# Kernel optimization log

Hardware: AMD Instinct MI355X
Metric: run time of the kernel (lower is better)

## Reference

```python
import jax, jax.numpy as jnp
import numpy as np

N, S_CT, D = 64, 128, 1024
WIN = 5
EPS = 1e-8
STOP = 0.1
MAX_DEPTH = 25


def layer_norm(x, g, b, eps=1e-5):
    mu = jnp.mean(x, axis=-1, keepdims=True)
    var = jnp.var(x, axis=-1, keepdims=True)
    return (x - mu) / jnp.sqrt(var + eps) * g + b


def _augment(sequence, input_mask, START, END):
    n, s, d = sequence.shape
    seq = jnp.concatenate([jnp.broadcast_to(START, (n, 1, d)), sequence], axis=1)
    m = jnp.concatenate([jnp.ones((n, 1, 1), seq.dtype), input_mask], axis=1)
    m_no_end = jnp.concatenate([m, jnp.zeros((n, 1, 1), seq.dtype)], axis=1)
    m_yes_end = jnp.concatenate([jnp.ones((n, 1, 1), seq.dtype), m], axis=1)
    end_mask = m_yes_end - m_no_end  # one-hot at END slot
    seq = jnp.concatenate([seq, jnp.zeros((n, 1, d), seq.dtype)], axis=1)
    seq = end_mask * END + (1.0 - end_mask) * seq
    m_no_start = jnp.concatenate([jnp.zeros((n, 1, 1), seq.dtype), m_yes_end[:, 1:]], axis=1)
    return seq, m_yes_end, end_mask, m_no_start, m_no_end


def _neighbor_probs(exist_probs, mask):
    # exist_probs, mask: (n,s,1). Returns left/right soft-neighbor matrices (n,s,s).
    n, s, _ = mask.shape
    m = jnp.stack([mask[:, ::-1, 0], mask[:, :, 0]], axis=1)            # (n,2,s)
    p = jnp.stack([exist_probs[:, ::-1, 0], exist_probs[:, :, 0]], axis=1)
    tri = jnp.triu(jnp.ones((s, s), mask.dtype), k=1)
    mat = (p * m)[:, :, None, :] * tri                                   # (n,2,s,s)
    cs = jnp.cumsum(mat, axis=-1)
    rem_left = jnp.concatenate([jnp.ones((n, 2, s, 1), mask.dtype), 1.0 - cs[..., :-1]], axis=-1)
    rem_left = jnp.maximum(rem_left, 0.0)
    right = jnp.where(cs > 1.0, rem_left, mat) * m[:, :, None, :]
    left = jnp.flip(right[:, 0], axis=(1, 2))
    return left, right[:, 1]


def crvnn_forward(sequence, input_mask, START, END, W_conv, b_conv, W_scorer, b_scorer,
                  W_init, b_init, W_cell1, b_cell1, W_cell2, b_cell2,
                  ln1_g, ln1_b, ln2_g, ln2_b):
    seq, mask, end_mask, m_no_start, m_no_end = _augment(sequence, input_mask, START, END)
    n, s, d = seq.shape
    last_mask = jnp.concatenate([end_mask[:, 1:], jnp.zeros((n, 1, 1), seq.dtype)], axis=1)
    sel_mask = m_no_start * m_no_end * (1.0 - last_mask)  # start_end_last_mask
    seq = layer_norm((seq * mask) @ W_init + b_init, ln1_g, ln1_b) * mask
    exist = jnp.ones((n, s, 1), seq.dtype) * mask

    def step(carry, _):
        sq, ep, um = carry
        L, R = _neighbor_probs(ep, mask)
        l1 = L @ sq; l2 = L @ l1
        r1 = R @ sq; r2 = R @ r1
        win = jnp.concatenate([l2, l1, sq, r1, r2], axis=-1)  # (n,s,5d) == stacked window flattened
        h = jax.nn.gelu(win @ W_conv + b_conv, approximate=False)
        sc = h @ W_scorer + b_scorer                           # (n,s,1) transition score
        scores = jnp.concatenate([sc, jnp.zeros_like(sc)], axis=-1)
        exp_scores = jnp.exp(scores - jnp.max(scores))
        exp_t = exp_scores[..., 0:1] * sel_mask
        exp_n = exp_scores[..., 1:2]
        # sum_normalize over {transition, no_op}; gate halted samples via um (tp=0 => no-op)
        tp = exp_t / (exp_t + exp_n + 2.0 * EPS) * um[:, None, None]
        # compose(left_child, self)
        cat = jnp.concatenate([l1, sq], axis=-1)
        hid = jax.nn.gelu(cat @ W_cell1 + b_cell1, approximate=False)
        contents = (hid @ W_cell2 + b_cell2).reshape(n, s, 4, d)
        gates = jax.nn.sigmoid(contents[:, :, 0:3, :])
        comp = layer_norm(gates[:, :, 0] * l1 + gates[:, :, 1] * sq + gates[:, :, 2] * contents[:, :, 3, :], ln2_g, ln2_b)
        new_sq = tp * comp + (1.0 - tp) * sq
        new_ep = ep * (1.0 - (R @ tp))  # left neighbor consumed with prob of right neighbor transition
        active = jnp.sum(new_ep * sel_mask, axis=(1, 2))
        new_um = um * (active >= STOP).astype(sq.dtype)
        return (new_sq, new_ep, new_um), None

    steps = min(s - 2, MAX_DEPTH)
    (seq, exist, _), _ = jax.lax.scan(step, (seq, exist, jnp.ones((n,), seq.dtype)), None, length=steps)
    seq = seq * mask
    global_state = jnp.sum(last_mask * seq, axis=1)  # root lands at last content slot
    return seq[:, 1:-1, :], global_state


def setup_inputs():
    key = jax.random.key(0)
    ks = jax.random.split(key, 8)
    sc = 0.02
    f32 = jnp.float32
    return {
        "sequence": jax.random.normal(ks[0], (N, S_CT, D), f32),
        "input_mask": jnp.ones((N, S_CT, 1), f32),
        "START": jax.random.normal(ks[1], (D,), f32),
        "END": jax.random.normal(ks[2], (D,), f32),
        "W_conv": jax.random.normal(ks[3], (WIN * D, D), f32) * sc,
        "b_conv": jnp.zeros((D,), f32),
        "W_scorer": jax.random.normal(ks[4], (D, 1), f32) * sc,
        "b_scorer": jnp.zeros((1,), f32),
        "W_init": jax.random.normal(ks[5], (D, D), f32) * sc,
        "b_init": jnp.zeros((D,), f32),
        "W_cell1": jax.random.normal(ks[6], (2 * D, 4 * D), f32) * sc,
        "b_cell1": jnp.zeros((4 * D,), f32),
        "W_cell2": jax.random.normal(ks[7], (4 * D, 4 * D), f32) * sc,
        "b_cell2": jnp.zeros((4 * D,), f32),
        "ln1_g": jnp.ones((D,), f32), "ln1_b": jnp.zeros((D,), f32),
        "ln2_g": jnp.ones((D,), f32), "ln2_b": jnp.zeros((D,), f32),
    }


def reference(sequence, input_mask, START, END, W_conv, b_conv, W_scorer, b_scorer,
              W_init, b_init, W_cell1, b_cell1, W_cell2, b_cell2,
              ln1_g, ln1_b, ln2_g, ln2_b):
    return crvnn_forward(sequence, input_mask, START, END, W_conv, b_conv, W_scorer, b_scorer,
                         W_init, b_init, W_cell1, b_cell1, W_cell2, b_cell2,
                         ln1_g, ln1_b, ln2_g, ln2_b)
```

## Files before the change

kernel.cpp:

```cpp
#include <hip/hip_runtime.h>
#include <math.h>


#define NB 64
#define SS 130
#define DD 1024
#define MM (NB*SS)
#define LSTR 132
#define CROWS 1664

typedef _Float16 f16x8 __attribute__((ext_vector_type(8)));
typedef _Float16 f16x4 __attribute__((ext_vector_type(4)));
typedef _Float16 f16x2 __attribute__((ext_vector_type(2)));
typedef float f32x4 __attribute__((ext_vector_type(4)));

struct GemmSrc { const float* a[5]; };

__device__ __forceinline__ float bsum(float v){
  __shared__ float sh[4];
  __syncthreads();
  #pragma unroll
  for (int o=32;o;o>>=1) v += __shfl_down(v,o);
  if ((threadIdx.x & 63)==0) sh[threadIdx.x>>6] = v;
  __syncthreads();
  return sh[0]+sh[1]+sh[2]+sh[3];
}
__device__ __forceinline__ float bmaxr(float v){
  __shared__ float sh[4];
  __syncthreads();
  #pragma unroll
  for (int o=32;o;o>>=1) v = fmaxf(v,__shfl_down(v,o));
  if ((threadIdx.x & 63)==0) sh[threadIdx.x>>6] = v;
  __syncthreads();
  return fmaxf(fmaxf(sh[0],sh[1]),fmaxf(sh[2],sh[3]));
}
__device__ __forceinline__ float gelu_(float x){
  return 0.5f*x*(1.f+erff(x*0.70710678118654752f));
}

__global__ __launch_bounds__(256) void build_masks(
    const float* __restrict__ im, float* __restrict__ mk, float* __restrict__ sel,
    float* __restrict__ lastm, float* __restrict__ endm, float* __restrict__ ep,
    float* __restrict__ um, int* __restrict__ flag){
  int b = blockIdx.x, i = threadIdx.x;
  if (i < SS){
    float mye = (i<=1) ? 1.f : im[b*128 + (i-2)];
    float mne = (i==SS-1) ? 0.f : ((i==0) ? 1.f : im[b*128 + (i-1)]);
    float em  = mye - mne;
    float mns = (i==0) ? 0.f : mye;
    float lm;
    if (i < SS-1){
      int i1 = i+1;
      float mye1 = (i1<=1) ? 1.f : im[b*128 + (i1-2)];
      float mne1 = (i1==SS-1) ? 0.f : im[b*128 + (i1-1)];
      lm = mye1 - mne1;
    } else lm = 0.f;
    float sl = mns * mne * (1.f - lm);
    int idx = b*SS + i;
    mk[idx]=mye; sel[idx]=sl; lastm[idx]=lm; endm[idx]=em; ep[idx]=mye;
  } else if (i == SS) { um[b] = 1.f; }
  else if (i == SS+1 && b==0) { flag[0] = 0; }
}

__global__ __launch_bounds__(256) void build_seq(
    const float* __restrict__ seqin, const float* __restrict__ START,
    const float* __restrict__ END, const float* __restrict__ mk,
    const float* __restrict__ endm, float* __restrict__ out){
  int r = blockIdx.x; int b = r/SS, i = r%SS; int t = threadIdx.x;
  float em = endm[r], m = mk[r];
  #pragma unroll
  for (int q=0;q<4;q++){
    int j = t + q*256;
    float v;
    if (i==0) v = START[j];
    else if (i<=128) v = seqin[((size_t)b*128 + (i-1))*DD + j];
    else v = 0.f;
    v = em*END[j] + (1.f-em)*v;
    out[(size_t)r*DD + j] = v*m;
  }
}

__global__ __launch_bounds__(256) void wtranspose(
    const float* __restrict__ W, _Float16* __restrict__ WTh, _Float16* __restrict__ WTl,
    int K, int N){
  __shared__ float Ts[32][33];
  int k0 = blockIdx.x*32, n0 = blockIdx.y*32;
  int t = threadIdx.x;
  int r = t>>3, c4 = (t&7)*4;
  float4 v = *(const float4*)(W + (size_t)(k0+r)*N + n0 + c4);
  Ts[r][c4]=v.x; Ts[r][c4+1]=v.y; Ts[r][c4+2]=v.z; Ts[r][c4+3]=v.w;
  __syncthreads();
  int n = t>>3, k4 = (t&7)*4;
  f16x4 h, lo;
  #pragma unroll
  for (int i=0;i<4;i++){
    float xs = Ts[k4+i][n] * 64.f;
    _Float16 hh = (_Float16)xs;
    h[i] = hh; lo[i] = (_Float16)((xs - (float)hh) * 2048.f);
  }
  *(f16x4*)(WTh + (size_t)(n0+n)*K + k0+k4) = h;
  *(f16x4*)(WTl + (size_t)(n0+n)*K + k0+k4) = lo;
}

template<bool PRE>
__global__ __launch_bounds__(256,2) void gemm_mfma(
    GemmSrc S, long lda,
    const _Float16* __restrict__ WTh, const _Float16* __restrict__ WTl,
    const float* __restrict__ Wf, int Nw,
    const float* __restrict__ bias,
    float* __restrict__ C, long ldc, int K, int act,
    const int* __restrict__ flag, float* __restrict__ spart, const float* __restrict__ Ws){
  if (flag[0]) return;
  __shared__ _Float16 Ah[128][40], Al[128][40];
  __shared__ _Float16 Wh[128][40], Wl[128][40];
  const int t = threadIdx.x;
  const int wave = t >> 6, lane = t & 63;
  const int wm = wave >> 1, wn = wave & 1;
  const int l15 = lane & 15, l4 = lane >> 4;
  int lin = blockIdx.y * gridDim.x + blockIdx.x;
  int nwg = gridDim.x * gridDim.y;
  int q = nwg >> 3, r = nwg & 7;
  int xcd = lin & 7, pos = lin >> 3;
  int wg = (xcd < r) ? (xcd*(q+1) + pos) : (r*(q+1) + (xcd - r)*q + pos);
  int MT = gridDim.y;
  int mt = wg % MT, nt = wg / MT;
  const long mb = (long)mt * 128;
  const int  nb = nt * 128;
  f32x4 accH[4][4], accX[4][4];
  #pragma unroll
  for (int i=0;i<4;i++)
    #pragma unroll
    for (int j=0;j<4;j++){ accH[i][j] = (f32x4){0.f,0.f,0.f,0.f}; accX[i][j] = (f32x4){0.f,0.f,0.f,0.f}; }

  for (int kt=0; kt<K; kt+=32){
    #pragma unroll
    for (int p=0;p<4;p++){
      int f = t + 256*p;
      int m = f >> 3;
      int k4 = (f & 7) * 4;
      int kg = kt + k4;
      const float* src = S.a[kg >> 10];
      float4 v = *(const float4*)(src + (mb + m)*lda + (kg & 1023));
      f16x4 h, lo;
      _Float16 hh;
      hh=(_Float16)v.x; h[0]=hh; lo[0]=(_Float16)((v.x-(float)hh)*2048.f);
      hh=(_Float16)v.y; h[1]=hh; lo[1]=(_Float16)((v.y-(float)hh)*2048.f);
      hh=(_Float16)v.z; h[2]=hh; lo[2]=(_Float16)((v.z-(float)hh)*2048.f);
      hh=(_Float16)v.w; h[3]=hh; lo[3]=(_Float16)((v.w-(float)hh)*2048.f);
      *(f16x4*)&Ah[m][k4] = h;
      *(f16x4*)&Al[m][k4] = lo;
    }
    if constexpr (PRE){
      #pragma unroll
      for (int p=0;p<2;p++){
        int f = t + 256*p;
        int n = f >> 2;
        int ko = (f & 3) * 8;
        *(f16x8*)&Wh[n][ko] = *(const f16x8*)(WTh + (size_t)(nb + n)*K + kt + ko);
        *(f16x8*)&Wl[n][ko] = *(const f16x8*)(WTl + (size_t)(nb + n)*K + kt + ko);
      }
    } else {
      #pragma unroll
      for (int p=0;p<2;p++){
        int u = t + 256*p;
        int kp = u >> 5;
        int c  = u & 31;
        const float* wsrc = Wf + (size_t)(kt + 2*kp)*Nw + nb + c;
        #pragma unroll
        for (int i=0;i<4;i++){
          float x0 = wsrc[32*i] * 64.f;
          float x1 = wsrc[(size_t)Nw + 32*i] * 64.f;
          _Float16 h0 = (_Float16)x0, h1 = (_Float16)x1;
          _Float16 g0 = (_Float16)((x0 - (float)h0)*2048.f);
          _Float16 g1 = (_Float16)((x1 - (float)h1)*2048.f);
          f16x2 hp; hp[0]=h0; hp[1]=h1;
          f16x2 lp; lp[0]=g0; lp[1]=g1;
          int n = c + 32*i;
          *(f16x2*)&Wh[n][2*kp] = hp;
          *(f16x2*)&Wl[n][2*kp] = lp;
        }
      }
    }
    __syncthreads();
    f16x8 wh[4], wl[4];
    #pragma unroll
    for (int i=0;i<4;i++){
      wh[i] = *(const f16x8*)&Wh[wn*64 + i*16 + l15][8*l4];
      wl[i] = *(const f16x8*)&Wl[wn*64 + i*16 + l15][8*l4];
    }
    #pragma unroll
    for (int mi=0;mi<4;mi++){
      f16x8 ahv = *(const f16x8*)&Ah[wm*64 + mi*16 + l15][8*l4];
      f16x8 alv = *(const f16x8*)&Al[wm*64 + mi*16 + l15][8*l4];
      #pragma unroll
      for (int ni=0;ni<4;ni++){
        accH[mi][ni] = __builtin_amdgcn_mfma_f32_16x16x32_f16(wh[ni], ahv, accH[mi][ni], 0,0,0);
        accX[mi][ni] = __builtin_amdgcn_mfma_f32_16x16x32_f16(wh[ni], alv, accX[mi][ni], 0,0,0);
        accX[mi][ni] = __builtin_amdgcn_mfma_f32_16x16x32_f16(wl[ni], ahv, accX[mi][ni], 0,0,0);
      }
    }
    __syncthreads();
  }

  const float IH = 1.f/64.f, IX = 1.f/131072.f;
  if (act==2){
    #pragma unroll
    for (int mi=0;mi<4;mi++){
      float s = 0.f;
      #pragma unroll
      for (int ni=0;ni<4;ni++){
        int nbase = nb + wn*64 + ni*16 + 4*l4;
        #pragma unroll
        for (int rr=0;rr<4;rr++){
          float v = gelu_(accH[mi][ni][rr]*IH + accX[mi][ni][rr]*IX + bias[nbase+rr]);
          s = fmaf(v, Ws[nbase+rr], s);
        }
      }
      s += __shfl_xor(s, 16);
      s += __shfl_xor(s, 32);
      if (l4==0){
        long m = mb + wm*64 + mi*16 + l15;
        spart[m*16 + nt*2 + wn] = s;
      }
    }
    return;
  }
  #pragma unroll
  for (int mi=0;mi<4;mi++){
    long m = mb + wm*64 + mi*16 + l15;
    #pragma unroll
    for (int ni=0;ni<4;ni++){
      int nbase = nb + wn*64 + ni*16 + 4*l4;
      float4 v;
      v.x = accH[mi][ni][0]*IH + accX[mi][ni][0]*IX + bias[nbase+0];
      v.y = accH[mi][ni][1]*IH + accX[mi][ni][1]*IX + bias[nbase+1];
      v.z = accH[mi][ni][2]*IH + accX[mi][ni][2]*IX + bias[nbase+2];
      v.w = accH[mi][ni][3]*IH + accX[mi][ni][3]*IX + bias[nbase+3];
      if (act==1){ v.x=gelu_(v.x); v.y=gelu_(v.y); v.z=gelu_(v.z); v.w=gelu_(v.w); }
      *(float4*)(C + m*ldc + nbase) = v;
    }
  }
}

__global__ __launch_bounds__(256,2) void gemm_f32(
    GemmSrc S, long lda, const float* __restrict__ B, const float* __restrict__ bias,
    float* __restrict__ C, long ldc, int N, int K, int act,
    const int* __restrict__ flag){
  if (flag[0]) return;
  __shared__ float Asm[16][132];
  __shared__ float Bsm[16][132];
  float acc[8][8];
  #pragma unroll
  for (int i=0;i<8;i++)
    #pragma unroll
    for (int j=0;j<8;j++) acc[i][j]=0.f;
  const int t = threadIdx.x;
  const int tx = t & 15, ty = t >> 4;
  const long mb = (long)blockIdx.y * 128;
  const int  nb = blockIdx.x * 128;
  for (int kt=0; kt<K; kt+=16){
    #pragma unroll
    for (int ii=0; ii<2; ii++){
      int f  = t + 256*ii;
      int m  = f >> 2;
      int k4 = (f & 3) * 4;
      int kg = kt + k4;
      const float* src = S.a[kg >> 10];
      float4 v = *(const float4*)(src + (mb + m)*lda + (kg & 1023));
      Asm[k4+0][m]=v.x; Asm[k4+1][m]=v.y; Asm[k4+2][m]=v.z; Asm[k4+3][m]=v.w;
    }
    #pragma unroll
    for (int ii=0; ii<2; ii++){
      int f  = t + 256*ii;
      int kk = f >> 5;
      int c4 = (f & 31)*4;
      *(float4*)&Bsm[kk][c4] = *(const float4*)(B + (long)(kt+kk)*N + nb + c4);
    }
    __syncthreads();
    #pragma unroll
    for (int kk=0;kk<16;kk++){
      float av[8], bv[8];
      *(float4*)&av[0] = *(const float4*)&Asm[kk][ty*4];
      *(float4*)&av[4] = *(const float4*)&Asm[kk][64+ty*4];
      *(float4*)&bv[0] = *(const float4*)&Bsm[kk][tx*4];
      *(float4*)&bv[4] = *(const float4*)&Bsm[kk][64+tx*4];
      #pragma unroll
      for (int r=0;r<8;r++)
        #pragma unroll
        for (int c=0;c<8;c++) acc[r][c] = fmaf(av[r],bv[c],acc[r][c]);
    }
    __syncthreads();
  }
  #pragma unroll
  for (int rh=0;rh<2;rh++)
  #pragma unroll
  for (int rr=0;rr<4;rr++){
    long row = mb + rh*64 + ty*4 + rr;
    #pragma unroll
    for (int ch=0;ch<2;ch++){
      int col = nb + ch*64 + tx*4;
      float t0 = acc[rh*4+rr][ch*4+0] + bias[col+0];
      float t1 = acc[rh*4+rr][ch*4+1] + bias[col+1];
      float t2 = acc[rh*4+rr][ch*4+2] + bias[col+2];
      float t3 = acc[rh*4+rr][ch*4+3] + bias[col+3];
      if (act==1){ t0=gelu_(t0); t1=gelu_(t1); t2=gelu_(t2); t3=gelu_(t3); }
      float4 v; v.x=t0; v.y=t1; v.z=t2; v.w=t3;
      *(float4*)(C + row*ldc + col) = v;
    }
  }
}

__global__ __launch_bounds__(256,2) void bgemm(
    const float* __restrict__ P, const float* __restrict__ X, float* __restrict__ Y,
    const int* __restrict__ flag){
  if (flag[0]) return;
  __shared__ float Ps[64][17];
  __shared__ float Xs[16][132];
  const int t = threadIdx.x;
  const int nt = blockIdx.x, mt = blockIdx.y, b = blockIdx.z;
  const int i0 = mt*64;
  const float* Pb = P + (size_t)b*SS*LSTR;
  const float* Xb = X + (size_t)b*SS*DD + nt*128;
  float* Yb = Y + (size_t)b*SS*DD + nt*128;
  const int tx = t & 7, ty = t >> 3;
  float acc[2][16];
  #pragma unroll
  for (int r=0;r<2;r++)
    #pragma unroll
    for (int c=0;c<16;c++) acc[r][c]=0.f;
  for (int j0=0;j0<SS;j0+=16){
    { int r = t>>2, c0 = (t&3)*4;
      float4 v = make_float4(0.f,0.f,0.f,0.f);
      if (i0 + r < SS && j0 + c0 < LSTR) v = *(const float4*)(Pb + (size_t)(i0+r)*LSTR + j0 + c0);
      Ps[r][c0]=v.x; Ps[r][c0+1]=v.y; Ps[r][c0+2]=v.z; Ps[r][c0+3]=v.w;
    }
    #pragma unroll
    for (int ii=0;ii<2;ii++){
      int f = t + 256*ii;
      int jj = f>>5, c4 = (f&31)*4;
      float4 v = make_float4(0.f,0.f,0.f,0.f);
      if (j0 + jj < SS) v = *(const float4*)(Xb + (size_t)(j0+jj)*DD + c4);
      *(float4*)&Xs[jj][c4] = v;
    }
    __syncthreads();
    #pragma unroll
    for (int jj=0;jj<16;jj++){
      float p0 = Ps[2*ty][jj], p1 = Ps[2*ty+1][jj];
      #pragma unroll
      for (int q=0;q<4;q++){
        float4 xv = *(const float4*)&Xs[jj][tx*4 + 32*q];
        acc[0][q*4+0] = fmaf(p0,xv.x,acc[0][q*4+0]);
        acc[0][q*4+1] = fmaf(p0,xv.y,acc[0][q*4+1]);
        acc[0][q*4+2] = fmaf(p0,xv.z,acc[0][q*4+2]);
        acc[0][q*4+3] = fmaf(p0,xv.w,acc[0][q*4+3]);
        acc[1][q*4+0] = fmaf(p1,xv.x,acc[1][q*4+0]);
        acc[1][q*4+1] = fmaf(p1,xv.y,acc[1][q*4+1]);
        acc[1][q*4+2] = fmaf(p1,xv.z,acc[1][q*4+2]);
        acc[1][q*4+3] = fmaf(p1,xv.w,acc[1][q*4+3]);
      }
    }
    __syncthreads();
  }
  #pragma unroll
  for (int rr=0;rr<2;rr++){
    int row = i0 + 2*ty + rr;
    if (row < SS){
      #pragma unroll
      for (int q=0;q<4;q++){
        float4 v = make_float4(acc[rr][q*4],acc[rr][q*4+1],acc[rr][q*4+2],acc[rr][q*4+3]);
        *(float4*)(Yb + (size_t)row*DD + tx*4 + 32*q) = v;
      }
    }
  }
}

__global__ void neighbor_kernel(const float* __restrict__ ep, const float* __restrict__ mk,
                                float* __restrict__ L, float* __restrict__ R,
                                const int* __restrict__ flag){
  if (flag[0]) return;
  int idx = blockIdx.x*blockDim.x + threadIdx.x;
  if (idx >= MM) return;
  int b = idx / SS, i = idx % SS;
  const float* p = ep + b*SS;
  const float* m = mk + b*SS;
  float* Lr = L + (size_t)idx*LSTR;
  float* Rr = R + (size_t)idx*LSTR;
  for (int j=0;j<LSTR;j++){ Lr[j]=0.f; Rr[j]=0.f; }
  float cs=0.f;
  for (int j=i+1;j<SS;j++){
    float mat = p[j]*m[j];
    cs += mat;
    float v = (cs>1.f) ? fmaxf(1.f-(cs-mat),0.f) : mat;
    Rr[j] = v*m[j];
  }
  cs=0.f;
  for (int j=i-1;j>=0;j--){
    float mat = p[j]*m[j];
    cs += mat;
    float v = (cs>1.f) ? fmaxf(1.f-(cs-mat),0.f) : mat;
    Lr[j] = v*m[j];
  }
}

__global__ __launch_bounds__(256) void ln1_kernel(
    const float* __restrict__ xin, const float* __restrict__ g, const float* __restrict__ bb,
    const float* __restrict__ mk, float* __restrict__ out){
  int r = blockIdx.x, t = threadIdx.x;
  const float* xr = xin + (size_t)r*DD;
  float x[4]; float s=0.f;
  #pragma unroll
  for (int q=0;q<4;q++){ x[q]=xr[t+256*q]; s+=x[q]; }
  float mean = bsum(s)*(1.f/DD);
  float vs=0.f;
  #pragma unroll
  for (int q=0;q<4;q++){ float d=x[q]-mean; vs+=d*d; }
  float var = bsum(vs)*(1.f/DD);
  float inv = 1.f/sqrtf(var+1e-5f);
  float m = mk[r];
  #pragma unroll
  for (int q=0;q<4;q++){ int j=t+256*q; out[(size_t)r*DD+j] = ((x[q]-mean)*inv*g[j]+bb[j])*m; }
}

__global__ void scorer_final(const float* __restrict__ spart, const float* __restrict__ bs,
                             float* __restrict__ sc, const int* __restrict__ flag){
  if (flag[0]) return;
  int r = blockIdx.x*blockDim.x + threadIdx.x;
  if (r >= MM) return;
  float s = bs[0];
  #pragma unroll
  for (int k=0;k<16;k++) s += spart[(size_t)r*16+k];
  sc[r] = s;
}
__global__ __launch_bounds__(256) void max1(const float* __restrict__ sc, float* __restrict__ part,
                                            const int* __restrict__ flag){
  if (flag[0]) return;
  int idx = blockIdx.x*256 + threadIdx.x;
  float v = -1e30f;
  for (int i = idx; i < MM; i += 64*256) v = fmaxf(v, sc[i]);
  v = bmaxr(v);
  if (threadIdx.x==0) part[blockIdx.x] = v;
}
__global__ __launch_bounds__(64) void max2(const float* __restrict__ part, float* __restrict__ gm,
                                           const int* __restrict__ flag){
  if (flag[0]) return;
  float v = part[threadIdx.x];
  #pragma unroll
  for (int o=32;o;o>>=1) v = fmaxf(v, __shfl_down(v,o));
  if (threadIdx.x==0) gm[0] = fmaxf(v, 0.f);
}
__global__ void tp_kernel(const float* __restrict__ sc, const float* __restrict__ sel,
                          const float* __restrict__ um, const float* __restrict__ gm,
                          float* __restrict__ tp, const int* __restrict__ flag){
  if (flag[0]) return;
  int idx = blockIdx.x*blockDim.x + threadIdx.x;
  if (idx>=MM) return;
  int b = idx / SS;
  float g = gm[0];
  float et = expf(sc[idx]-g)*sel[idx];
  float en = expf(-g);
  tp[idx] = et/(et+en+2e-8f)*um[b];
}

__global__ __launch_bounds__(256) void update_kernel(
    const float* __restrict__ cont, const float* __restrict__ l1, float* __restrict__ sq,
    const float* __restrict__ tp, const float* __restrict__ g, const float* __restrict__ bb,
    const int* __restrict__ flag, long row0){
  if (flag[0]) return;
  long r = row0 + blockIdx.x; int t = threadIdx.x;
  const float* cr = cont + (size_t)blockIdx.x*4096;
  const float* lr = l1 + (size_t)r*DD;
  float* sr = sq + (size_t)r*DD;
  float x[4], sv[4];
  float s=0.f;
  #pragma unroll
  for (int q=0;q<4;q++){
    int j = t+q*256;
    float c0=cr[j], c1=cr[DD+j], c2=cr[2*DD+j], c3=cr[3*DD+j];
    float g0=1.f/(1.f+expf(-c0));
    float g1=1.f/(1.f+expf(-c1));
    float g2=1.f/(1.f+expf(-c2));
    float lv=lr[j]; float sqv=sr[j]; sv[q]=sqv;
    x[q] = g0*lv + g1*sqv + g2*c3;
    s += x[q];
  }
  float mean = bsum(s)*(1.f/DD);
  float vs=0.f;
  #pragma unroll
  for (int q=0;q<4;q++){ float d=x[q]-mean; vs+=d*d; }
  float var = bsum(vs)*(1.f/DD);
  float inv = 1.f/sqrtf(var+1e-5f);
  float tpv = tp[r];
  #pragma unroll
  for (int q=0;q<4;q++){
    int j=t+q*256;
    float comp = (x[q]-mean)*inv*g[j]+bb[j];
    sr[j] = tpv*comp + (1.f-tpv)*sv[q];
  }
}

__global__ void ep_update(float* __restrict__ ep, const float* __restrict__ R,
                          const float* __restrict__ tp, const int* __restrict__ flag){
  if (flag[0]) return;
  int idx = blockIdx.x*blockDim.x + threadIdx.x;
  if (idx>=MM) return;
  int b = idx / SS;
  const float* Rr = R + (size_t)idx*LSTR;
  const float* tb = tp + b*SS;
  float d=0.f;
  for (int j=0;j<SS;j++) d = fmaf(Rr[j],tb[j],d);
  ep[idx] *= (1.f - d);
}
__global__ __launch_bounds__(256) void active_um(const float* __restrict__ ep,
                                                 const float* __restrict__ sel,
                                                 float* __restrict__ um,
                                                 const int* __restrict__ flag){
  if (flag[0]) return;
  int b = blockIdx.x, t = threadIdx.x;
  float s = (t<SS) ? ep[b*SS+t]*sel[b*SS+t] : 0.f;
  s = bsum(s);
  if (t==0) um[b] *= (s >= 0.1f) ? 1.f : 0.f;
}
__global__ __launch_bounds__(64) void done_kernel(const float* __restrict__ um, int* __restrict__ flag){
  float v = um[threadIdx.x];
  unsigned long long b = __ballot(v > 0.f);
  if (threadIdx.x==0) flag[0] = (b==0ULL) ? 1 : 0;
}

__global__ __launch_bounds__(256) void output_kernel(const float* __restrict__ sq,
                                                     const float* __restrict__ mk,
                                                     float* __restrict__ out){
  int r = blockIdx.x; int b = r/SS, i = r%SS;
  if (i<1 || i>128) return;
  float m = mk[r]; int t=threadIdx.x;
  #pragma unroll
  for (int q=0;q<4;q++){
    int j = t+q*256;
    out[((size_t)b*128 + (i-1))*DD + j] = sq[(size_t)r*DD + j]*m;
  }
}
__global__ __launch_bounds__(256) void gstate_kernel(const float* __restrict__ sq,
                                                     const float* __restrict__ mk,
                                                     const float* __restrict__ lastm,
                                                     float* __restrict__ outg){
  int b = blockIdx.x; int t=threadIdx.x;
  #pragma unroll
  for (int q=0;q<4;q++){
    int j = t+q*256;
    float acc=0.f;
    for (int i=0;i<SS;i++){
      float w = lastm[b*SS+i]*mk[b*SS+i];
      acc = fmaf(w, sq[((size_t)(b*SS+i))*DD + j], acc);
    }
    outg[(size_t)b*DD + j] = acc;
  }
}

extern "C" void kernel_launch(void* const* d_in, const int* in_sizes, int n_in,
                              void* d_out, int out_size, void* d_ws, size_t ws_size,
                              hipStream_t stream) {
  const float* sequence   = (const float*)d_in[0];
  const float* input_mask = (const float*)d_in[1];
  const float* START      = (const float*)d_in[2];
  const float* END        = (const float*)d_in[3];
  const float* W_conv     = (const float*)d_in[4];
  const float* b_conv     = (const float*)d_in[5];
  const float* W_scorer   = (const float*)d_in[6];
  const float* b_scorer   = (const float*)d_in[7];
  const float* W_init     = (const float*)d_in[8];
  const float* b_init     = (const float*)d_in[9];
  const float* W_cell1    = (const float*)d_in[10];
  const float* b_cell1    = (const float*)d_in[11];
  const float* W_cell2    = (const float*)d_in[12];
  const float* b_cell2    = (const float*)d_in[13];
  const float* ln1g       = (const float*)d_in[14];
  const float* ln1b       = (const float*)d_in[15];
  const float* ln2g       = (const float*)d_in[16];
  const float* ln2b       = (const float*)d_in[17];

  float* ws = (float*)d_ws;
  const size_t U = (size_t)MM*DD;
  float* sq   = ws;
  float* l1   = ws + U;
  float* r1   = ws + 2*U;
  float* l2   = ws + 3*U;
  float* r2   = ws + 4*U;
  float* Lm   = ws + 5*U;
  float* Rm   = Lm + (size_t)NB*SS*LSTR;
  float* maskv= Rm + (size_t)NB*SS*LSTR;
  float* sel  = maskv + MM;
  float* lastm= sel + MM;
  float* endm = lastm + MM;
  float* ep   = endm + MM;
  float* scb  = ep + MM;
  float* tpb  = scb + MM;
  float* spart= tpb + MM;
  float* umb  = spart + (size_t)MM*16;
  float* part = umb + NB;
  float* gmx  = part + 64;
  int*   flag = (int*)(gmx + 4);
  size_t used_floats = (size_t)((float*)(flag+4) - ws);
  used_floats = (used_floats + 7) & ~(size_t)7;
  const size_t SC = (size_t)1024*5120, S1 = (size_t)4096*2048, S2 = (size_t)4096*4096;
  _Float16* WT2_h = (_Float16*)(ws + used_floats);
  _Float16* WT2_l = WT2_h + S2;
  _Float16* WT1_h = WT2_l + S2;
  _Float16* WT1_l = WT1_h + S1;
  _Float16* WTc_h = WT1_l + S1;
  _Float16* WTc_l = WTc_h + SC;
  const bool pre2 = ws_size >= (size_t)((char*)(WT2_l + S2) - (char*)d_ws);
  const bool pre1 = ws_size >= (size_t)((char*)(WT1_l + S1) - (char*)d_ws);
  const bool prec = ws_size >= (size_t)((char*)(WTc_l + SC) - (char*)d_ws);

  build_masks<<<NB,256,0,stream>>>(input_mask, maskv, sel, lastm, endm, ep, umb, flag);
  build_seq<<<MM,256,0,stream>>>(sequence, START, END, maskv, endm, r1);
  GemmSrc si; si.a[0]=r1; si.a[1]=r1; si.a[2]=r1; si.a[3]=r1; si.a[4]=r1;
  gemm_f32<<<dim3(8,65),256,0,stream>>>(si, DD, W_init, b_init, l2, DD, DD, DD, 0, flag);
  ln1_kernel<<<MM,256,0,stream>>>(l2, ln1g, ln1b, maskv, sq);

  if (pre2) wtranspose<<<dim3(128,128),256,0,stream>>>(W_cell2, WT2_h, WT2_l, 4096, 4096);
  if (pre1) wtranspose<<<dim3(64,128),256,0,stream>>>(W_cell1, WT1_h, WT1_l, 2048, 4096);
  if (prec) wtranspose<<<dim3(160,32),256,0,stream>>>(W_conv,  WTc_h, WTc_l, 5120, 1024);

  for (int it=0; it<25; ++it){
    neighbor_kernel<<<(MM+255)/256,256,0,stream>>>(ep, maskv, Lm, Rm, flag);
    bgemm<<<dim3(8,3,NB),256,0,stream>>>(Lm, sq, l1, flag);
    bgemm<<<dim3(8,3,NB),256,0,stream>>>(Rm, sq, r1, flag);
    bgemm<<<dim3(8,3,NB),256,0,stream>>>(Lm, l1, l2, flag);
    bgemm<<<dim3(8,3,NB),256,0,stream>>>(Rm, r1, r2, flag);
    GemmSrc s5; s5.a[0]=l2; s5.a[1]=l1; s5.a[2]=sq; s5.a[3]=r1; s5.a[4]=r2;
    if (prec)
      gemm_mfma<true ><<<dim3(8,65),256,0,stream>>>(s5, DD, WTc_h, WTc_l, nullptr, 0, b_conv, nullptr, 0, 5120, 2, flag, spart, W_scorer);
    else
      gemm_mfma<false><<<dim3(8,65),256,0,stream>>>(s5, DD, nullptr, nullptr, W_conv, 1024, b_conv, nullptr, 0, 5120, 2, flag, spart, W_scorer);
    scorer_final<<<(MM+255)/256,256,0,stream>>>(spart, b_scorer, scb, flag);
    max1<<<64,256,0,stream>>>(scb, part, flag);
    max2<<<1,64,0,stream>>>(part, gmx, flag);
    tp_kernel<<<(MM+255)/256,256,0,stream>>>(scb, sel, umb, gmx, tpb, flag);
    for (int c=0;c<5;c++){
      long row0 = (long)c*CROWS;
      GemmSrc s2; s2.a[0]=l1+row0*DD; s2.a[1]=sq+row0*DD; s2.a[2]=s2.a[1]; s2.a[3]=s2.a[1]; s2.a[4]=s2.a[1];
      GemmSrc s3; s3.a[0]=l2; s3.a[1]=l2+DD; s3.a[2]=l2+2*DD; s3.a[3]=l2+3*DD; s3.a[4]=l2;
      if (pre1)
        gemm_mfma<true ><<<dim3(32,13),256,0,stream>>>(s2, DD,   WT1_h, WT1_l, nullptr, 0, b_cell1, l2, 4096, 2048, 1, flag, nullptr, nullptr);
      else
        gemm_mfma<false><<<dim3(32,13),256,0,stream>>>(s2, DD,   nullptr, nullptr, W_cell1, 4096, b_cell1, l2, 4096, 2048, 1, flag, nullptr, nullptr);
      if (pre2)
        gemm_mfma<true ><<<dim3(32,13),256,0,stream>>>(s3, 4096, WT2_h, WT2_l, nullptr, 0, b_cell2, r2, 4096, 4096, 0, flag, nullptr, nullptr);
      else
        gemm_mfma<false><<<dim3(32,13),256,0,stream>>>(s3, 4096, nullptr, nullptr, W_cell2, 4096, b_cell2, r2, 4096, 4096, 0, flag, nullptr, nullptr);
      update_kernel<<<CROWS,256,0,stream>>>(r2, l1, sq, tpb, ln2g, ln2b, flag, row0);
    }
    ep_update<<<(MM+255)/256,256,0,stream>>>(ep, Rm, tpb, flag);
    active_um<<<NB,256,0,stream>>>(ep, sel, umb, flag);
    done_kernel<<<1,64,0,stream>>>(umb, flag);
  }

  float* out = (float*)d_out;
  output_kernel<<<MM,256,0,stream>>>(sq, maskv, out);
  gstate_kernel<<<NB,256,0,stream>>>(sq, maskv, lastm, out + (size_t)NB*128*DD);
}
```

Measured before the change: 67.42 ms.

## Store activations as pre-split fp16 hi/lo pairs and parallelize neighbor/ep kernels

Intermediate activations (sq, l1, r1, l2, r2) are now kept as split fp16 high/low pairs, so the MFMA GEMMs load them straight into shared memory instead of converting fp32 to hi/lo on every K tile. Producers (ln1, bgemm, cell1 GEMM epilogue, update) encode on write, and consumers decode where fp32 is still needed. Separately, neighbor_kernel and ep_update now use one wave per row with shuffle prefix sums and reductions, replacing the serial per-thread loops. The split encoding should keep accuracy close to fp32, but it adds encode/decode work in the bgemm, update and output kernels.

```diff
diff --git a/kernel.cpp b/kernel.cpp
--- a/kernel.cpp
+++ b/kernel.cpp
@@ -8,13 +8,17 @@
 #define MM (NB*SS)
 #define LSTR 132
 #define CROWS 1664
+#define RSC 2048.0f
+#define IRS (1.0f/2048.0f)
 
 typedef _Float16 f16x8 __attribute__((ext_vector_type(8)));
 typedef _Float16 f16x4 __attribute__((ext_vector_type(4)));
 typedef _Float16 f16x2 __attribute__((ext_vector_type(2)));
 typedef float f32x4 __attribute__((ext_vector_type(4)));
 
-struct GemmSrc { const float* a[5]; };
+struct GemmSrcF { const float* a[5]; };
+struct GemmSrcP { const _Float16* h[5]; const _Float16* l[5]; };
+struct hl2 { _Float16 h, l; };
 
 __device__ __forceinline__ float bsum(float v){
   __shared__ float sh[4];
@@ -36,6 +40,12 @@
 }
 __device__ __forceinline__ float gelu_(float x){
   return 0.5f*x*(1.f+erff(x*0.70710678118654752f));
+}
+__device__ __forceinline__ hl2 enc(float x){
+  hl2 r;
+  r.h = (_Float16)x;
+  r.l = (_Float16)((x - (float)r.h)*RSC);
+  return r;
 }
 
 __global__ __launch_bounds__(256) void build_masks(
@@ -94,21 +104,21 @@
   f16x4 h, lo;
   #pragma unroll
   for (int i=0;i<4;i++){
-    float xs = Ts[k4+i][n] * 64.f;
-    _Float16 hh = (_Float16)xs;
-    h[i] = hh; lo[i] = (_Float16)((xs - (float)hh) * 2048.f);
+    hl2 e = enc(Ts[k4+i][n] * 64.f);
+    h[i] = e.h; lo[i] = e.l;
   }
   *(f16x4*)(WTh + (size_t)(n0+n)*K + k0+k4) = h;
   *(f16x4*)(WTl + (size_t)(n0+n)*K + k0+k4) = lo;
 }
 
-template<bool PRE>
+template<bool PREW>
 __global__ __launch_bounds__(256,2) void gemm_mfma(
-    GemmSrc S, long lda,
+    GemmSrcP S, long lda,
     const _Float16* __restrict__ WTh, const _Float16* __restrict__ WTl,
     const float* __restrict__ Wf, int Nw,
     const float* __restrict__ bias,
-    float* __restrict__ C, long ldc, int K, int act,
+    float* __restrict__ C, _Float16* __restrict__ Ch, _Float16* __restrict__ Cl,
+    long ldc, int K, int act,
     const int* __restrict__ flag, float* __restrict__ spart, const float* __restrict__ Ws){
   if (flag[0]) return;
   __shared__ _Float16 Ah[128][40], Al[128][40];
@@ -134,23 +144,17 @@
 
   for (int kt=0; kt<K; kt+=32){
     #pragma unroll
-    for (int p=0;p<4;p++){
+    for (int p=0;p<2;p++){
       int f = t + 256*p;
-      int m = f >> 3;
-      int k4 = (f & 7) * 4;
-      int kg = kt + k4;
-      const float* src = S.a[kg >> 10];
-      float4 v = *(const float4*)(src + (mb + m)*lda + (kg & 1023));
-      f16x4 h, lo;
-      _Float16 hh;
-      hh=(_Float16)v.x; h[0]=hh; lo[0]=(_Float16)((v.x-(float)hh)*2048.f);
-      hh=(_Float16)v.y; h[1]=hh; lo[1]=(_Float16)((v.y-(float)hh)*2048.f);
-      hh=(_Float16)v.z; h[2]=hh; lo[2]=(_Float16)((v.z-(float)hh)*2048.f);
-      hh=(_Float16)v.w; h[3]=hh; lo[3]=(_Float16)((v.w-(float)hh)*2048.f);
-      *(f16x4*)&Ah[m][k4] = h;
-      *(f16x4*)&Al[m][k4] = lo;
-    }
-    if constexpr (PRE){
+      int m = f >> 2;
+      int ko = (f & 3) * 8;
+      int kg = kt + ko;
+      const _Float16* sh = S.h[kg >> 10];
+      const _Float16* sl = S.l[kg >> 10];
+      *(f16x8*)&Ah[m][ko] = *(const f16x8*)(sh + (mb + m)*lda + (kg & 1023));
+      *(f16x8*)&Al[m][ko] = *(const f16x8*)(sl + (mb + m)*lda + (kg & 1023));
+    }
+    if constexpr (PREW){
       #pragma unroll
       for (int p=0;p<2;p++){
         int f = t + 256*p;
@@ -168,13 +172,10 @@
         const float* wsrc = Wf + (size_t)(kt + 2*kp)*Nw + nb + c;
         #pragma unroll
         for (int i=0;i<4;i++){
-          float x0 = wsrc[32*i] * 64.f;
-          float x1 = wsrc[(size_t)Nw + 32*i] * 64.f;
-          _Float16 h0 = (_Float16)x0, h1 = (_Float16)x1;
-          _Float16 g0 = (_Float16)((x0 - (float)h0)*2048.f);
-          _Float16 g1 = (_Float16)((x1 - (float)h1)*2048.f);
-          f16x2 hp; hp[0]=h0; hp[1]=h1;
-          f16x2 lp; lp[0]=g0; lp[1]=g1;
+          hl2 e0 = enc(wsrc[32*i] * 64.f);
+          hl2 e1 = enc(wsrc[(size_t)Nw + 32*i] * 64.f);
+          f16x2 hp; hp[0]=e0.h; hp[1]=e1.h;
+          f16x2 lp; lp[0]=e0.l; lp[1]=e1.l;
           int n = c + 32*i;
           *(f16x2*)&Wh[n][2*kp] = hp;
           *(f16x2*)&Wl[n][2*kp] = lp;
@@ -231,19 +232,27 @@
     #pragma unroll
     for (int ni=0;ni<4;ni++){
       int nbase = nb + wn*64 + ni*16 + 4*l4;
-      float4 v;
-      v.x = accH[mi][ni][0]*IH + accX[mi][ni][0]*IX + bias[nbase+0];
-      v.y = accH[mi][ni][1]*IH + accX[mi][ni][1]*IX + bias[nbase+1];
-      v.z = accH[mi][ni][2]*IH + accX[mi][ni][2]*IX + bias[nbase+2];
-      v.w = accH[mi][ni][3]*IH + accX[mi][ni][3]*IX + bias[nbase+3];
-      if (act==1){ v.x=gelu_(v.x); v.y=gelu_(v.y); v.z=gelu_(v.z); v.w=gelu_(v.w); }
-      *(float4*)(C + m*ldc + nbase) = v;
+      float v0 = accH[mi][ni][0]*IH + accX[mi][ni][0]*IX + bias[nbase+0];
+      float v1 = accH[mi][ni][1]*IH + accX[mi][ni][1]*IX + bias[nbase+1];
+      float v2 = accH[mi][ni][2]*IH + accX[mi][ni][2]*IX + bias[nbase+2];
+      float v3 = accH[mi][ni][3]*IH + accX[mi][ni][3]*IX + bias[nbase+3];
+      if (act==1){
+        v0=gelu_(v0); v1=gelu_(v1); v2=gelu_(v2); v3=gelu_(v3);
+        hl2 e0=enc(v0), e1=enc(v1), e2=enc(v2), e3=enc(v3);
+        f16x4 h4; h4[0]=e0.h; h4[1]=e1.h; h4[2]=e2.h; h4[3]=e3.h;
+        f16x4 l4v; l4v[0]=e0.l; l4v[1]=e1.l; l4v[2]=e2.l; l4v[3]=e3.l;
+        *(f16x4*)(Ch + m*ldc + nbase) = h4;
+        *(f16x4*)(Cl + m*ldc + nbase) = l4v;
+      } else {
+        float4 v; v.x=v0; v.y=v1; v.z=v2; v.w=v3;
+        *(float4*)(C + m*ldc + nbase) = v;
+      }
     }
   }
 }
 
 __global__ __launch_bounds__(256,2) void gemm_f32(
-    GemmSrc S, long lda, const float* __restrict__ B, const float* __restrict__ bias,
+    GemmSrcF S, long lda, const float* __restrict__ B, const float* __restrict__ bias,
     float* __restrict__ C, long ldc, int N, int K, int act,
     const int* __restrict__ flag){
   if (flag[0]) return;
@@ -299,19 +308,20 @@
     #pragma unroll
     for (int ch=0;ch<2;ch++){
       int col = nb + ch*64 + tx*4;
-      float t0 = acc[rh*4+rr][ch*4+0] + bias[col+0];
-      float t1 = acc[rh*4+rr][ch*4+1] + bias[col+1];
-      float t2 = acc[rh*4+rr][ch*4+2] + bias[col+2];
-      float t3 = acc[rh*4+rr][ch*4+3] + bias[col+3];
-      if (act==1){ t0=gelu_(t0); t1=gelu_(t1); t2=gelu_(t2); t3=gelu_(t3); }
-      float4 v; v.x=t0; v.y=t1; v.z=t2; v.w=t3;
+      float4 v;
+      v.x = acc[rh*4+rr][ch*4+0] + bias[col+0];
+      v.y = acc[rh*4+rr][ch*4+1] + bias[col+1];
+      v.z = acc[rh*4+rr][ch*4+2] + bias[col+2];
+      v.w = acc[rh*4+rr][ch*4+3] + bias[col+3];
       *(float4*)(C + row*ldc + col) = v;
     }
   }
 }
 
 __global__ __launch_bounds__(256,2) void bgemm(
-    const float* __restrict__ P, const float* __restrict__ X, float* __restrict__ Y,
+    const float* __restrict__ P,
+    const _Float16* __restrict__ Xh, const _Float16* __restrict__ Xl,
+    _Float16* __restrict__ Yh, _Float16* __restrict__ Yl,
     const int* __restrict__ flag){
   if (flag[0]) return;
   __shared__ float Ps[64][17];
@@ -320,8 +330,10 @@
   const int nt = blockIdx.x, mt = blockIdx.y, b = blockIdx.z;
   const int i0 = mt*64;
   const float* Pb = P + (size_t)b*SS*LSTR;
-  const float* Xb = X + (size_t)b*SS*DD + nt*128;
-  float* Yb = Y + (size_t)b*SS*DD + nt*128;
+  const _Float16* Xhb = Xh + (size_t)b*SS*DD + nt*128;
+  const _Float16* Xlb = Xl + (size_t)b*SS*DD + nt*128;
+  _Float16* Yhb = Yh + (size_t)b*SS*DD + nt*128;
+  _Float16* Ylb = Yl + (size_t)b*SS*DD + nt*128;
   const int tx = t & 7, ty = t >> 3;
   float acc[2][16];
   #pragma unroll
@@ -338,9 +350,16 @@
     for (int ii=0;ii<2;ii++){
       int f = t + 256*ii;
       int jj = f>>5, c4 = (f&31)*4;
-      float4 v = make_float4(0.f,0.f,0.f,0.f);
-      if (j0 + jj < SS) v = *(const float4*)(Xb + (size_t)(j0+jj)*DD + c4);
-      *(float4*)&Xs[jj][c4] = v;
+      float x0=0.f,x1=0.f,x2=0.f,x3=0.f;
+      if (j0 + jj < SS){
+        f16x4 xh = *(const f16x4*)(Xhb + (size_t)(j0+jj)*DD + c4);
+        f16x4 xl = *(const f16x4*)(Xlb + (size_t)(j0+jj)*DD + c4);
+        x0 = (float)xh[0] + (float)xl[0]*IRS;
+        x1 = (float)xh[1] + (float)xl[1]*IRS;
+        x2 = (float)xh[2] + (float)xl[2]*IRS;
+        x3 = (float)xh[3] + (float)xl[3]*IRS;
+      }
+      Xs[jj][c4]=x0; Xs[jj][c4+1]=x1; Xs[jj][c4+2]=x2; Xs[jj][c4+3]=x3;
     }
     __syncthreads();
     #pragma unroll
@@ -367,44 +386,78 @@
     if (row < SS){
       #pragma unroll
       for (int q=0;q<4;q++){
-        float4 v = make_float4(acc[rr][q*4],acc[rr][q*4+1],acc[rr][q*4+2],acc[rr][q*4+3]);
-        *(float4*)(Yb + (size_t)row*DD + tx*4 + 32*q) = v;
-      }
-    }
-  }
-}
-
-__global__ void neighbor_kernel(const float* __restrict__ ep, const float* __restrict__ mk,
-                                float* __restrict__ L, float* __restrict__ R,
-                                const int* __restrict__ flag){
-  if (flag[0]) return;
-  int idx = blockIdx.x*blockDim.x + threadIdx.x;
+        hl2 e0 = enc(acc[rr][q*4+0]);
+        hl2 e1 = enc(acc[rr][q*4+1]);
+        hl2 e2 = enc(acc[rr][q*4+2]);
+        hl2 e3 = enc(acc[rr][q*4+3]);
+        f16x4 h4; h4[0]=e0.h; h4[1]=e1.h; h4[2]=e2.h; h4[3]=e3.h;
+        f16x4 l4v; l4v[0]=e0.l; l4v[1]=e1.l; l4v[2]=e2.l; l4v[3]=e3.l;
+        *(f16x4*)(Yhb + (size_t)row*DD + tx*4 + 32*q) = h4;
+        *(f16x4*)(Ylb + (size_t)row*DD + tx*4 + 32*q) = l4v;
+      }
+    }
+  }
+}
+
+__global__ __launch_bounds__(256) void neighbor_kernel(
+    const float* __restrict__ ep, const float* __restrict__ mk,
+    float* __restrict__ L, float* __restrict__ R, const int* __restrict__ flag){
+  if (flag[0]) return;
+  int wave = threadIdx.x >> 6, lane = threadIdx.x & 63;
+  int idx = blockIdx.x*4 + wave;
   if (idx >= MM) return;
   int b = idx / SS, i = idx % SS;
   const float* p = ep + b*SS;
   const float* m = mk + b*SS;
+  float mR[3], mL[3], mv[3];
+  #pragma unroll
+  for (int c=0;c<3;c++){
+    int j = lane + 64*c;
+    float pj = (j<SS)? p[j] : 0.f;
+    float mj = (j<SS)? m[j] : 0.f;
+    mv[c] = mj;
+    float x = pj*mj;
+    mR[c] = (j>i)? x : 0.f;
+    mL[c] = (j<i)? x : 0.f;
+  }
+  float csR[3]; float run = 0.f;
+  #pragma unroll
+  for (int c=0;c<3;c++){
+    float s = mR[c];
+    #pragma unroll
+    for (int o=1;o<64;o<<=1){ float v = __shfl_up(s,o); if (lane>=o) s += v; }
+    csR[c] = s + run;
+    run += __shfl(s,63);
+  }
+  float csL[3]; run = 0.f;
+  #pragma unroll
+  for (int cc=0;cc<3;cc++){
+    int c = 2-cc;
+    float s = mL[c];
+    #pragma unroll
+    for (int o=1;o<64;o<<=1){ float v = __shfl_down(s,o); if (lane < 64-o) s += v; }
+    csL[c] = s + run;
+    run += __shfl(s,0);
+  }
   float* Lr = L + (size_t)idx*LSTR;
   float* Rr = R + (size_t)idx*LSTR;
-  for (int j=0;j<LSTR;j++){ Lr[j]=0.f; Rr[j]=0.f; }
-  float cs=0.f;
-  for (int j=i+1;j<SS;j++){
-    float mat = p[j]*m[j];
-    cs += mat;
-    float v = (cs>1.f) ? fmaxf(1.f-(cs-mat),0.f) : mat;
-    Rr[j] = v*m[j];
-  }
-  cs=0.f;
-  for (int j=i-1;j>=0;j--){
-    float mat = p[j]*m[j];
-    cs += mat;
-    float v = (cs>1.f) ? fmaxf(1.f-(cs-mat),0.f) : mat;
-    Lr[j] = v*m[j];
+  #pragma unroll
+  for (int c=0;c<3;c++){
+    int j = lane + 64*c;
+    if (j < LSTR){
+      float rv = 0.f, lv = 0.f;
+      if (j < SS){
+        rv = ((csR[c]>1.f) ? fmaxf(1.f-(csR[c]-mR[c]),0.f) : mR[c]) * mv[c];
+        lv = ((csL[c]>1.f) ? fmaxf(1.f-(csL[c]-mL[c]),0.f) : mL[c]) * mv[c];
+      }
+      Rr[j] = rv; Lr[j] = lv;
+    }
   }
 }
 
 __global__ __launch_bounds__(256) void ln1_kernel(
     const float* __restrict__ xin, const float* __restrict__ g, const float* __restrict__ bb,
-    const float* __restrict__ mk, float* __restrict__ out){
+    const float* __restrict__ mk, _Float16* __restrict__ sqh, _Float16* __restrict__ sql){
   int r = blockIdx.x, t = threadIdx.x;
   const float* xr = xin + (size_t)r*DD;
   float x[4]; float s=0.f;
@@ -418,7 +471,12 @@
   float inv = 1.f/sqrtf(var+1e-5f);
   float m = mk[r];
   #pragma unroll
-  for (int q=0;q<4;q++){ int j=t+256*q; out[(size_t)r*DD+j] = ((x[q]-mean)*inv*g[j]+bb[j])*m; }
+  for (int q=0;q<4;q++){
+    int j=t+256*q;
+    float v = ((x[q]-mean)*inv*g[j]+bb[j])*m;
+    hl2 e = enc(v);
+    sqh[(size_t)r*DD+j] = e.h; sql[(size_t)r*DD+j] = e.l;
+  }
 }
 
 __global__ void scorer_final(const float* __restrict__ spart, const float* __restrict__ bs,
@@ -462,14 +520,18 @@
 }
 
 __global__ __launch_bounds__(256) void update_kernel(
-    const float* __restrict__ cont, const float* __restrict__ l1, float* __restrict__ sq,
+    const float* __restrict__ cont,
+    const _Float16* __restrict__ l1h, const _Float16* __restrict__ l1l,
+    _Float16* __restrict__ sqh, _Float16* __restrict__ sql,
     const float* __restrict__ tp, const float* __restrict__ g, const float* __restrict__ bb,
     const int* __restrict__ flag, long row0){
   if (flag[0]) return;
   long r = row0 + blockIdx.x; int t = threadIdx.x;
   const float* cr = cont + (size_t)blockIdx.x*4096;
-  const float* lr = l1 + (size_t)r*DD;
-  float* sr = sq + (size_t)r*DD;
+  const _Float16* lh = l1h + (size_t)r*DD;
+  const _Float16* ll = l1l + (size_t)r*DD;
+  _Float16* sh = sqh + (size_t)r*DD;
+  _Float16* sl = sql + (size_t)r*DD;
   float x[4], sv[4];
   float s=0.f;
   #pragma unroll
@@ -479,7 +541,9 @@
     float g0=1.f/(1.f+expf(-c0));
     float g1=1.f/(1.f+expf(-c1));
     float g2=1.f/(1.f+expf(-c2));
-    float lv=lr[j]; float sqv=sr[j]; sv[q]=sqv;
+    float lv = (float)lh[j] + (float)ll[j]*IRS;
+    float sqv = (float)sh[j] + (float)sl[j]*IRS;
+    sv[q]=sqv;
     x[q] = g0*lv + g1*sqv + g2*c3;
     s += x[q];
   }
@@ -494,22 +558,33 @@
   for (int q=0;q<4;q++){
     int j=t+q*256;
     float comp = (x[q]-mean)*inv*g[j]+bb[j];
-    sr[j] = tpv*comp + (1.f-tpv)*sv[q];
-  }
-}
-
-__global__ void ep_update(float* __restrict__ ep, const float* __restrict__ R,
-                          const float* __restrict__ tp, const int* __restrict__ flag){
-  if (flag[0]) return;
-  int idx = blockIdx.x*blockDim.x + threadIdx.x;
-  if (idx>=MM) return;
+    float out = tpv*comp + (1.f-tpv)*sv[q];
+    hl2 e = enc(out);
+    sh[j]=e.h; sl[j]=e.l;
+  }
+}
+
+__global__ __launch_bounds__(256) void ep_update(
+    float* __restrict__ ep, const float* __restrict__ R,
+    const float* __restrict__ tp, const int* __restrict__ flag){
+  if (flag[0]) return;
+  int wave = threadIdx.x >> 6, lane = threadIdx.x & 63;
+  int idx = blockIdx.x*4 + wave;
+  if (idx >= MM) return;
   int b = idx / SS;
   const float* Rr = R + (size_t)idx*LSTR;
   const float* tb = tp + b*SS;
-  float d=0.f;
-  for (int j=0;j<SS;j++) d = fmaf(Rr[j],tb[j],d);
-  ep[idx] *= (1.f - d);
-}
+  float d = 0.f;
+  #pragma unroll
+  for (int c=0;c<3;c++){
+    int j = lane + 64*c;
+    if (j < SS) d = fmaf(Rr[j], tb[j], d);
+  }
+  #pragma unroll
+  for (int o=32;o;o>>=1) d += __shfl_xor(d,o);
+  if (lane==0) ep[idx] *= (1.f - d);
+}
+
 __global__ __launch_bounds__(256) void active_um(const float* __restrict__ ep,
                                                  const float* __restrict__ sel,
                                                  float* __restrict__ um,
@@ -526,22 +601,23 @@
   if (threadIdx.x==0) flag[0] = (b==0ULL) ? 1 : 0;
 }
 
-__global__ __launch_bounds__(256) void output_kernel(const float* __restrict__ sq,
-                                                     const float* __restrict__ mk,
-                                                     float* __restrict__ out){
+__global__ __launch_bounds__(256) void output_kernel(
+    const _Float16* __restrict__ sqh, const _Float16* __restrict__ sql,
+    const float* __restrict__ mk, float* __restrict__ out){
   int r = blockIdx.x; int b = r/SS, i = r%SS;
   if (i<1 || i>128) return;
   float m = mk[r]; int t=threadIdx.x;
   #pragma unroll
   for (int q=0;q<4;q++){
     int j = t+q*256;
-    out[((size_t)b*128 + (i-1))*DD + j] = sq[(size_t)r*DD + j]*m;
-  }
-}
-__global__ __launch_bounds__(256) void gstate_kernel(const float* __restrict__ sq,
-                                                     const float* __restrict__ mk,
-                                                     const float* __restrict__ lastm,
-                                                     float* __restrict__ outg){
+    float v = (float)sqh[(size_t)r*DD+j] + (float)sql[(size_t)r*DD+j]*IRS;
+    out[((size_t)b*128 + (i-1))*DD + j] = v*m;
+  }
+}
+__global__ __launch_bounds__(256) void gstate_kernel(
+    const _Float16* __restrict__ sqh, const _Float16* __restrict__ sql,
+    const float* __restrict__ mk, const float* __restrict__ lastm,
+    float* __restrict__ outg){
   int b = blockIdx.x; int t=threadIdx.x;
   #pragma unroll
   for (int q=0;q<4;q++){
@@ -549,7 +625,9 @@
     float acc=0.f;
     for (int i=0;i<SS;i++){
       float w = lastm[b*SS+i]*mk[b*SS+i];
-      acc = fmaf(w, sq[((size_t)(b*SS+i))*DD + j], acc);
+      size_t o = ((size_t)(b*SS+i))*DD + j;
+      float v = (float)sqh[o] + (float)sql[o]*IRS;
+      acc = fmaf(w, v, acc);
     }
     outg[(size_t)b*DD + j] = acc;
   }
@@ -579,11 +657,14 @@
 
   float* ws = (float*)d_ws;
   const size_t U = (size_t)MM*DD;
-  float* sq   = ws;
-  float* l1   = ws + U;
-  float* r1   = ws + 2*U;
-  float* l2   = ws + 3*U;
-  float* r2   = ws + 4*U;
+  _Float16* sq_h = (_Float16*)(ws);        _Float16* sq_l = sq_h + U;
+  _Float16* l1_h = (_Float16*)(ws + U);    _Float16* l1_l = l1_h + U;
+  _Float16* r1_h = (_Float16*)(ws + 2*U);  _Float16* r1_l = r1_h + U;
+  _Float16* l2_h = (_Float16*)(ws + 3*U);  _Float16* l2_l = l2_h + U;
+  _Float16* r2_h = (_Float16*)(ws + 4*U);  _Float16* r2_l = r2_h + U;
+  float* contb = ws + 4*U;
+  float* seqtmp  = ws + U;
+  float* inittmp = ws + 2*U;
   float* Lm   = ws + 5*U;
   float* Rm   = Lm + (size_t)NB*SS*LSTR;
   float* maskv= Rm + (size_t)NB*SS*LSTR;
@@ -612,50 +693,57 @@
   const bool prec = ws_size >= (size_t)((char*)(WTc_l + SC) - (char*)d_ws);
 
   build_masks<<<NB,256,0,stream>>>(input_mask, maskv, sel, lastm, endm, ep, umb, flag);
-  build_seq<<<MM,256,0,stream>>>(sequence, START, END, maskv, endm, r1);
-  GemmSrc si; si.a[0]=r1; si.a[1]=r1; si.a[2]=r1; si.a[3]=r1; si.a[4]=r1;
-  gemm_f32<<<dim3(8,65),256,0,stream>>>(si, DD, W_init, b_init, l2, DD, DD, DD, 0, flag);
-  ln1_kernel<<<MM,256,0,stream>>>(l2, ln1g, ln1b, maskv, sq);
+  build_seq<<<MM,256,0,stream>>>(sequence, START, END, maskv, endm, seqtmp);
+  GemmSrcF si; si.a[0]=seqtmp; si.a[1]=seqtmp; si.a[2]=seqtmp; si.a[3]=seqtmp; si.a[4]=seqtmp;
+  gemm_f32<<<dim3(8,65),256,0,stream>>>(si, DD, W_init, b_init, inittmp, DD, DD, DD, 0, flag);
+  ln1_kernel<<<MM,256,0,stream>>>(inittmp, ln1g, ln1b, maskv, sq_h, sq_l);
 
   if (pre2) wtranspose<<<dim3(128,128),256,0,stream>>>(W_cell2, WT2_h, WT2_l, 4096, 4096);
   if (pre1) wtranspose<<<dim3(64,128),256,0,stream>>>(W_cell1, WT1_h, WT1_l, 2048, 4096);
   if (prec) wtranspose<<<dim3(160,32),256,0,stream>>>(W_conv,  WTc_h, WTc_l, 5120, 1024);
 
+  const int NBLK = (MM + 3) / 4;
   for (int it=0; it<25; ++it){
-    neighbor_kernel<<<(MM+255)/256,256,0,stream>>>(ep, maskv, Lm, Rm, flag);
-    bgemm<<<dim3(8,3,NB),256,0,stream>>>(Lm, sq, l1, flag);
-    bgemm<<<dim3(8,3,NB),256,0,stream>>>(Rm, sq, r1, flag);
-    bgemm<<<dim3(8,3,NB),256,0,stream>>>(Lm, l1, l2, flag);
-    bgemm<<<dim3(8,3,NB),256,0,stream>>>(Rm, r1, r2, flag);
-    GemmSrc s5; s5.a[0]=l2; s5.a[1]=l1; s5.a[2]=sq; s5.a[3]=r1; s5.a[4]=r2;
+    neighbor_kernel<<<NBLK,256,0,stream>>>(ep, maskv, Lm, Rm, flag);
+    bgemm<<<dim3(8,3,NB),256,0,stream>>>(Lm, sq_h, sq_l, l1_h, l1_l, flag);
+    bgemm<<<dim3(8,3,NB),256,0,stream>>>(Rm, sq_h, sq_l, r1_h, r1_l, flag);
+    bgemm<<<dim3(8,3,NB),256,0,stream>>>(Lm, l1_h, l1_l, l2_h, l2_l, flag);
+    bgemm<<<dim3(8,3,NB),256,0,stream>>>(Rm, r1_h, r1_l, r2_h, r2_l, flag);
+    GemmSrcP s5;
+    s5.h[0]=l2_h; s5.h[1]=l1_h; s5.h[2]=sq_h; s5.h[3]=r1_h; s5.h[4]=r2_h;
+    s5.l[0]=l2_l; s5.l[1]=l1_l; s5.l[2]=sq_l; s5.l[3]=r1_l; s5.l[4]=r2_l;
     if (prec)
-      gemm_mfma<true ><<<dim3(8,65),256,0,stream>>>(s5, DD, WTc_h, WTc_l, nullptr, 0, b_conv, nullptr, 0, 5120, 2, flag, spart, W_scorer);
+      gemm_mfma<true ><<<dim3(8,65),256,0,stream>>>(s5, DD, WTc_h, WTc_l, nullptr, 0, b_conv, nullptr, nullptr, nullptr, 0, 5120, 2, flag, spart, W_scorer);
     else
-      gemm_mfma<false><<<dim3(8,65),256,0,stream>>>(s5, DD, nullptr, nullptr, W_conv, 1024, b_conv, nullptr, 0, 5120, 2, flag, spart, W_scorer);
+      gemm_mfma<false><<<dim3(8,65),256,0,stream>>>(s5, DD, nullptr, nullptr, W_conv, 1024, b_conv, nullptr, nullptr, nullptr, 0, 5120, 2, flag, spart, W_scorer);
     scorer_final<<<(MM+255)/256,256,0,stream>>>(spart, b_scorer, scb, flag);
     max1<<<64,256,0,stream>>>(scb, part, flag);
     max2<<<1,64,0,stream>>>(part, gmx, flag);
     tp_kernel<<<(MM+255)/256,256,0,stream>>>(scb, sel, umb, gmx, tpb, flag);
     for (int c=0;c<5;c++){
       long row0 = (long)c*CROWS;
-      GemmSrc s2; s2.a[0]=l1+row0*DD; s2.a[1]=sq+row0*DD; s2.a[2]=s2.a[1]; s2.a[3]=s2.a[1]; s2.a[4]=s2.a[1];
-      GemmSrc s3; s3.a[0]=l2; s3.a[1]=l2+DD; s3.a[2]=l2+2*DD; s3.a[3]=l2+3*DD; s3.a[4]=l2;
+      GemmSrcP s2;
+      s2.h[0]=l1_h+row0*DD; s2.h[1]=sq_h+row0*DD; s2.h[2]=s2.h[1]; s2.h[3]=s2.h[1]; s2.h[4]=s2.h[1];
+      s2.l[0]=l1_l+row0*DD; s2.l[1]=sq_l+row0*DD; s2.l[2]=s2.l[1]; s2.l[3]=s2.l[1]; s2.l[4]=s2.l[1];
+      GemmSrcP s3;
+      s3.h[0]=l2_h; s3.h[1]=l2_h+DD; s3.h[2]=l2_h+2*DD; s3.h[3]=l2_h+3*DD; s3.h[4]=l2_h;
+      s3.l[0]=l2_l; s3.l[1]=l2_l+DD; s3.l[2]=l2_l+2*DD; s3.l[3]=l2_l+3*DD; s3.l[4]=l2_l;
       if (pre1)
-        gemm_mfma<true ><<<dim3(32,13),256,0,stream>>>(s2, DD,   WT1_h, WT1_l, nullptr, 0, b_cell1, l2, 4096, 2048, 1, flag, nullptr, nullptr);
+        gemm_mfma<true ><<<dim3(32,13),256,0,stream>>>(s2, DD,   WT1_h, WT1_l, nullptr, 0, b_cell1, nullptr, l2_h, l2_l, 4096, 2048, 1, flag, nullptr, nullptr);
       else
-        gemm_mfma<false><<<dim3(32,13),256,0,stream>>>(s2, DD,   nullptr, nullptr, W_cell1, 4096, b_cell1, l2, 4096, 2048, 1, flag, nullptr, nullptr);
+        gemm_mfma<false><<<dim3(32,13),256,0,stream>>>(s2, DD,   nullptr, nullptr, W_cell1, 4096, b_cell1, nullptr, l2_h, l2_l, 4096, 2048, 1, flag, nullptr, nullptr);
       if (pre2)
-        gemm_mfma<true ><<<dim3(32,13),256,0,stream>>>(s3, 4096, WT2_h, WT2_l, nullptr, 0, b_cell2, r2, 4096, 4096, 0, flag, nullptr, nullptr);
+        gemm_mfma<true ><<<dim3(32,13),256,0,stream>>>(s3, 4096, WT2_h, WT2_l, nullptr, 0, b_cell2, contb, nullptr, nullptr, 4096, 4096, 0, flag, nullptr, nullptr);
       else
-        gemm_mfma<false><<<dim3(32,13),256,0,stream>>>(s3, 4096, nullptr, nullptr, W_cell2, 4096, b_cell2, r2, 4096, 4096, 0, flag, nullptr, nullptr);
-      update_kernel<<<CROWS,256,0,stream>>>(r2, l1, sq, tpb, ln2g, ln2b, flag, row0);
-    }
-    ep_update<<<(MM+255)/256,256,0,stream>>>(ep, Rm, tpb, flag);
+        gemm_mfma<false><<<dim3(32,13),256,0,stream>>>(s3, 4096, nullptr, nullptr, W_cell2, 4096, b_cell2, contb, nullptr, nullptr, 4096, 4096, 0, flag, nullptr, nullptr);
+      update_kernel<<<CROWS,256,0,stream>>>(contb, l1_h, l1_l, sq_h, sq_l, tpb, ln2g, ln2b, flag, row0);
+    }
+    ep_update<<<NBLK,256,0,stream>>>(ep, Rm, tpb, flag);
     active_um<<<NB,256,0,stream>>>(ep, sel, umb, flag);
     done_kernel<<<1,64,0,stream>>>(umb, flag);
   }
 
   float* out = (float*)d_out;
-  output_kernel<<<MM,256,0,stream>>>(sq, maskv, out);
-  gstate_kernel<<<NB,256,0,stream>>>(sq, maskv, lastm, out + (size_t)NB*128*DD);
-}
+  output_kernel<<<MM,256,0,stream>>>(sq_h, sq_l, maskv, out);
+  gstate_kernel<<<NB,256,0,stream>>>(sq_h, sq_l, maskv, lastm, out + (size_t)NB*128*DD);
+}
```

New measurement: 63.81 ms. 5.3% less time.
